# Kernel tuning notes

Hardware: AMD Instinct MI355X
Metric: run time of the kernel (lower is better)

The kernel has to match this reference:

```python
import jax, jax.numpy as jnp
import numpy as np

FEAT = 256
NUM_ATOMS = np.array([2048, 1536, 1024, 2048, 512, 1792, 1280, 2048], dtype=np.int32)
B = len(NUM_ATOMS)
N = int(NUM_ATOMS.sum())          # 12288 total atoms
MAXN = int(NUM_ATOMS.max())       # 2048
# Static segment bookkeeping (num_atoms is structural, not data)
_OFFSETS = np.concatenate([[0], np.cumsum(NUM_ATOMS)[:-1]])
SEG = np.repeat(np.arange(B), NUM_ATOMS)            # [N] graph id per atom
POS = np.arange(N) - _OFFSETS[SEG]                  # [N] position within graph
VALID = np.arange(MAXN)[None, :] < NUM_ATOMS[:, None]  # [B, MAXN] key mask


def setup_inputs() -> dict:
    key = jax.random.key(0)
    k1, k2 = jax.random.split(key)
    s = jax.random.normal(k1, (N, FEAT), jnp.float32)
    # dense: feat_dim -> 3*feat_dim, with bias
    W = jax.random.normal(k2, (FEAT, 3 * FEAT), jnp.float32) / np.float32(np.sqrt(FEAT))
    b = jnp.zeros((3 * FEAT,), jnp.float32)
    num_atoms = jnp.asarray(NUM_ATOMS)
    return {"s": s, "W": W, "b": b, "num_atoms": num_atoms}


def _pad(X):
    # scatter flat [N, FEAT] atoms into padded [B, MAXN, FEAT]
    return jnp.zeros((B, MAXN, FEAT), X.dtype).at[SEG, POS].set(X)


def reference(s, W, b, num_atoms):
    qkv = s @ W + b                          # [N, 3*FEAT]
    Q, K, V = jnp.split(qkv, 3, axis=-1)     # each [N, FEAT]
    Qp, Kp, Vp = _pad(Q), _pad(K), _pad(V)   # [B, MAXN, FEAT]
    scale = np.float32(1.0 / np.sqrt(FEAT))
    scores = jnp.einsum('bqd,bkd->bqk', Qp, Kp) * scale   # [B, MAXN, MAXN]
    scores = jnp.where(VALID[:, None, :], scores, -jnp.inf)  # mask padded keys
    att = jax.nn.softmax(scores, axis=-1)
    out = jnp.einsum('bqk,bkd->bqd', att, Vp)             # [B, MAXN, FEAT]
    return out[SEG, POS]                                   # back to flat [N, FEAT]
```

## Files before the change

### kernel.cpp

```cpp
#include <hip/hip_runtime.h>

typedef __attribute__((ext_vector_type(8))) short short8;
typedef __attribute__((ext_vector_type(4))) short s16x4;
typedef __attribute__((ext_vector_type(4))) float f32x4;

#define MFMA16(a,b,c) __builtin_amdgcn_mfma_f32_16x16x32_bf16((a),(b),(c),0,0,0)

__device__ __forceinline__ ushort f2bf(float f){ union{float f; unsigned u;} v; v.f=f; unsigned r=v.u + 0x7fffu + ((v.u>>16)&1u); return (ushort)(r>>16); }
__device__ __forceinline__ float bf2f(ushort u){ union{unsigned u; float f;} v; v.u = ((unsigned)u)<<16; return v.f; }

__global__ void __launch_bounds__(256) prep(const float* __restrict__ S,
    ushort* __restrict__ Sb, const float* __restrict__ W, ushort* __restrict__ Wt)
{
    __shared__ __align__(16) ushort tile[64*72];
    const int t = threadIdx.x;
    if (blockIdx.x < 1024){
        const int tid = blockIdx.x*256 + t;
#pragma unroll
        for (int r=0;r<3;r++){
            const int idx = tid + r*262144;
            f32x4 v = ((const f32x4*)S)[idx];
            s16x4 o;
            o[0]=(short)f2bf(v[0]); o[1]=(short)f2bf(v[1]);
            o[2]=(short)f2bf(v[2]); o[3]=(short)f2bf(v[3]);
            ((s16x4*)Sb)[idx] = o;
        }
    } else {
        const int i = blockIdx.x - 1024;
        const int r0 = (i&3)*64, c0 = (i>>2)*64;
        const int rr = t>>2, g = (t&3)*16;
        const float* sp = W + (size_t)(r0+rr)*768 + c0 + g;
#pragma unroll
        for (int j=0;j<16;j++) tile[(g+j)*72 + rr] = f2bf(sp[j]);
        __syncthreads();
        ushort* dp = Wt + (size_t)(c0+rr)*256 + r0 + g;
        *(short8*)dp     = *(const short8*)&tile[rr*72 + g];
        *(short8*)(dp+8) = *(const short8*)&tile[rr*72 + g + 8];
    }
}

__global__ void __launch_bounds__(256) qkv_gemm(const ushort* __restrict__ Sb,
    const ushort* __restrict__ Wt, const float* __restrict__ bias,
    ushort* __restrict__ Q, ushort* __restrict__ K, ushort* __restrict__ Vt)
{
    __shared__ __align__(16) ushort Bl[64*264];
    const int t = threadIdx.x, w = t>>6, l = t&63, lr = l&15, lq = l>>4;
    const int m0 = blockIdx.x*128, n0 = blockIdx.y*64;

#pragma unroll
    for (int s=0;s<8;s++){
        const int u = t + s*256, row = u>>5, c8 = u&31;
        *(short8*)&Bl[row*264 + c8*8] = *(const short8*)(Wt + (size_t)(n0+row)*256 + c8*8);
    }
    __syncthreads();

    if (n0 < 512){
        f32x4 acc[2][4];
#pragma unroll
        for (int a=0;a<2;a++)
#pragma unroll
            for (int b2=0;b2<4;b2++) acc[a][b2]=(f32x4){0.f,0.f,0.f,0.f};
        const ushort* ap = Sb + (size_t)(m0 + w*32 + lr)*256 + lq*8;
#pragma unroll
        for (int kc=0;kc<8;kc++){
            short8 af0 = *(const short8*)(ap + kc*32);
            short8 af1 = *(const short8*)(ap + 16*256 + kc*32);
#pragma unroll
            for (int nt=0;nt<4;nt++){
                short8 bf = *(const short8*)&Bl[(nt*16+lr)*264 + lq*8 + kc*32];
                acc[0][nt] = MFMA16(af0, bf, acc[0][nt]);
                acc[1][nt] = MFMA16(af1, bf, acc[1][nt]);
            }
        }
        ushort* dst = (n0 < 256) ? Q : K;
        const int colbase = n0 & 255;
#pragma unroll
        for (int nt=0;nt<4;nt++){
            float bv = bias[n0 + nt*16 + lr];
#pragma unroll
            for (int mt=0;mt<2;mt++){
                const int row = m0 + w*32 + mt*16 + lq*4;
                ushort* o = dst + (size_t)row*256 + colbase + nt*16 + lr;
#pragma unroll
                for (int i=0;i<4;i++) o[(size_t)i*256] = f2bf(acc[mt][nt][i] + bv);
            }
        }
    } else {
        const int f0 = n0 - 512;
        f32x4 acc[4][2];
#pragma unroll
        for (int a=0;a<4;a++)
#pragma unroll
            for (int b2=0;b2<2;b2++) acc[a][b2]=(f32x4){0.f,0.f,0.f,0.f};
        const ushort* bp = Sb + (size_t)(m0 + w*32 + lr)*256 + lq*8;
#pragma unroll
        for (int kc=0;kc<8;kc++){
            short8 bf0 = *(const short8*)(bp + kc*32);
            short8 bf1 = *(const short8*)(bp + 16*256 + kc*32);
#pragma unroll
            for (int ft=0;ft<4;ft++){
                short8 af = *(const short8*)&Bl[(ft*16+lr)*264 + lq*8 + kc*32];
                acc[ft][0] = MFMA16(af, bf0, acc[ft][0]);
                acc[ft][1] = MFMA16(af, bf1, acc[ft][1]);
            }
        }
#pragma unroll
        for (int ft=0;ft<4;ft++){
#pragma unroll
            for (int at=0;at<2;at++){
                ushort* o = Vt + (size_t)(f0 + ft*16 + lq*4)*12288 + m0 + w*32 + at*16 + lr;
#pragma unroll
                for (int i=0;i<4;i++){
                    float bv = bias[512 + f0 + ft*16 + lq*4 + i];
                    o[(size_t)i*12288] = f2bf(acc[ft][at][i] + bv);
                }
            }
        }
    }
}

template<int MODE>
__global__ void __launch_bounds__(256,2) attn_partial(const ushort* __restrict__ Qb,
    const ushort* __restrict__ Kb, const ushort* __restrict__ Vt,
    void* __restrict__ Optr, float* __restrict__ Lptr)
{
    __shared__ __align__(16) ushort Kl[32*264];
    __shared__ __align__(16) ushort Vl[256*40];
    __shared__ __align__(16) ushort Pl[4][32*40];
    const int t = threadIdx.x, w = t>>6, l = t&63, lr = l&15, lq = l>>4;

    const int offs[9]    = {0,2048,3584,4608,6656,7168,8960,10240,12288};
    const int pbase_t[8] = {0,8192,12800,14848,23040,23552,30720,34560};
    int bi = blockIdx.x, q0=0, kstart=0, kend=0, off=0, nbg=0, pbase=0;
#pragma unroll
    for (int s=0;s<8;s++){
        const int nb = offs[s+1]-offs[s];
        const int tiles = nb>>7, pieces = (nb+511)>>9;
        const int items = tiles*pieces;
        if (bi >= 0 && bi < items){
            const int tile = bi / pieces, piece = bi - tile*pieces;
            q0 = offs[s] + tile*128;
            kstart = offs[s] + piece*512;
            kend = min(offs[s]+nb, kstart+512);
            off = offs[s]; nbg = nb; pbase = pbase_t[s];
        }
        bi -= items;
    }
    const int nchunks = (kend - kstart) >> 5;
    const int pc = (kstart - off) >> 9;

    short8 qf[2][8];
#pragma unroll
    for (int g=0;g<2;g++){
        const ushort* qp = Qb + (size_t)(q0 + w*32 + g*16 + lr)*256 + lq*8;
#pragma unroll
        for (int kc=0;kc<8;kc++) qf[g][kc] = *(const short8*)(qp + kc*32);
    }
    f32x4 Oa[2][16];
#pragma unroll
    for (int g=0;g<2;g++)
#pragma unroll
        for (int ft=0;ft<16;ft++) Oa[g][ft] = (f32x4){0.f,0.f,0.f,0.f};
    float l_lane[2][4] = {{0.f,0.f,0.f,0.f},{0.f,0.f,0.f,0.f}};

    const int kr = t>>5, kcol = t&31;
    const ushort* kg0 = Kb + (size_t)(kstart + kr)*256 + kcol*8;
    const ushort* vg0 = Vt + (size_t)t*12288 + kstart;
    short8 kreg[4], vreg[4];
#pragma unroll
    for (int s=0;s<4;s++){
        kreg[s] = *(const short8*)(kg0 + (size_t)s*8*256);
        vreg[s] = *(const short8*)(vg0 + s*8);
    }

    for (int ck=0; ck<nchunks; ck++){
#pragma unroll
        for (int s=0;s<4;s++)
            *(short8*)&Kl[(kr + s*8)*264 + kcol*8] = kreg[s];
#pragma unroll
        for (int s=0;s<4;s++)
            *(short8*)&Vl[t*40 + s*8] = vreg[s];
        if (ck+1 < nchunks){
            const ushort* kg = kg0 + (size_t)(ck+1)*32*256;
            const ushort* vg = vg0 + (ck+1)*32;
#pragma unroll
            for (int s=0;s<4;s++){
                kreg[s] = *(const short8*)(kg + (size_t)s*8*256);
                vreg[s] = *(const short8*)(vg + s*8);
            }
        }
        __asm__ volatile("s_waitcnt lgkmcnt(0)" ::: "memory");
        __builtin_amdgcn_s_barrier();

        f32x4 sc[2][2];
#pragma unroll
        for (int g=0;g<2;g++)
#pragma unroll
            for (int h=0;h<2;h++) sc[g][h] = (f32x4){0.f,0.f,0.f,0.f};
        __builtin_amdgcn_s_setprio(1);
#pragma unroll
        for (int kc=0;kc<8;kc++){
            short8 b0 = *(const short8*)&Kl[ lr     *264 + kc*32 + lq*8];
            short8 b1 = *(const short8*)&Kl[(16+lr)*264 + kc*32 + lq*8];
#pragma unroll
            for (int g=0;g<2;g++){
                sc[g][0] = MFMA16(qf[g][kc], b0, sc[g][0]);
                sc[g][1] = MFMA16(qf[g][kc], b1, sc[g][1]);
            }
        }
        __builtin_amdgcn_s_setprio(0);
        ushort* pw = &Pl[w][0];
#pragma unroll
        for (int g=0;g<2;g++)
#pragma unroll
            for (int i=0;i<4;i++){
                float p0 = exp2f(sc[g][0][i]*0.0901684284f);
                float p1 = exp2f(sc[g][1][i]*0.0901684284f);
                l_lane[g][i] += p0 + p1;
                pw[(g*16+lq*4+i)*40 + lr]      = f2bf(p0);
                pw[(g*16+lq*4+i)*40 + 16 + lr] = f2bf(p1);
            }
        __asm__ volatile("s_waitcnt lgkmcnt(0)" ::: "memory");
        short8 pf0 = *(const short8*)&pw[ lr     *40 + lq*8];
        short8 pf1 = *(const short8*)&pw[(16+lr)*40 + lq*8];

        __builtin_amdgcn_s_setprio(1);
#pragma unroll
        for (int ft=0;ft<16;ft++){
            short8 vf = *(const short8*)&Vl[(ft*16+lr)*40 + lq*8];
            Oa[0][ft] = MFMA16(pf0, vf, Oa[0][ft]);
            Oa[1][ft] = MFMA16(pf1, vf, Oa[1][ft]);
        }
        __builtin_amdgcn_s_setprio(0);
        __builtin_amdgcn_s_barrier();
    }

#pragma unroll
    for (int g=0;g<2;g++)
#pragma unroll
        for (int i=0;i<4;i++){
            float r = l_lane[g][i];
            r += __shfl_xor(r,1); r += __shfl_xor(r,2);
            r += __shfl_xor(r,4); r += __shfl_xor(r,8);
            l_lane[g][i] = r;
        }

    if constexpr (MODE == 0){
        ushort* Op = (ushort*)Optr;
        const int prow0 = pbase + pc*nbg + (q0 + w*32 - off);
#pragma unroll
        for (int g=0;g<2;g++)
#pragma unroll
            for (int i=0;i<4;i++){
                ushort* o = Op + (size_t)(prow0 + g*16 + lq*4 + i)*256 + lr;
#pragma unroll
                for (int ft=0;ft<16;ft++) o[ft*16] = f2bf(Oa[g][ft][i]);
            }
        if (lr == 0){
#pragma unroll
            for (int g=0;g<2;g++)
#pragma unroll
                for (int i=0;i<4;i++)
                    Lptr[prow0 + g*16 + lq*4 + i] = l_lane[g][i];
        }
    } else {
        float* out = (float*)Optr;
#pragma unroll
        for (int g=0;g<2;g++){
            float* op = out + (size_t)(q0 + w*32 + g*16 + lq*4)*256 + lr;
#pragma unroll
            for (int i=0;i<4;i++)
#pragma unroll
                for (int ft=0;ft<16;ft++)
                    atomicAdd(&op[(size_t)i*256 + ft*16], Oa[g][ft][i]);
        }
        if (lr == 0){
#pragma unroll
            for (int g=0;g<2;g++)
#pragma unroll
                for (int i=0;i<4;i++)
                    atomicAdd(&Lptr[q0 + w*32 + g*16 + lq*4 + i], l_lane[g][i]);
        }
    }
}

__global__ void __launch_bounds__(256) reduce_norm(const ushort* __restrict__ Opart,
    const float* __restrict__ Lpart, float* __restrict__ out)
{
    const int offs[9]    = {0,2048,3584,4608,6656,7168,8960,10240,12288};
    const int pbase_t[8] = {0,8192,12800,14848,23040,23552,30720,34560};
    const int pieces_t[8]= {4,3,2,4,1,4,3,4};
    const int t = threadIdx.x;
    const int row = blockIdx.x*8 + (t>>5);
    const int f = (t&31)*8;
    int s = 0;
#pragma unroll
    for (int i=0;i<8;i++) if (row >= offs[i+1]) s = i+1;
    const int nb = offs[s+1]-offs[s], S = pieces_t[s];
    const int base = pbase_t[s] + (row - offs[s]);
    float acc[8] = {0.f,0.f,0.f,0.f,0.f,0.f,0.f,0.f};
    float L = 0.f;
    for (int p=0; p<S; p++){
        const size_t pr = (size_t)(base + p*nb);
        L += Lpart[pr];
        short8 v = *(const short8*)&Opart[pr*256 + f];
#pragma unroll
        for (int j=0;j<8;j++) acc[j] += bf2f((ushort)v[j]);
    }
    const float inv = 1.0f / L;
    f32x4 o0, o1;
#pragma unroll
    for (int j=0;j<4;j++){ o0[j] = acc[j]*inv; o1[j] = acc[4+j]*inv; }
    float* op = out + (size_t)row*256 + f;
    *(f32x4*)op     = o0;
    *(f32x4*)(op+4) = o1;
}

__global__ void __launch_bounds__(256) normalize_out(float* __restrict__ out,
    const float* __restrict__ lsum)
{
    const int row = blockIdx.x, t = threadIdx.x;
    const float inv = 1.0f / lsum[row];
    out[(size_t)row*256 + t] *= inv;
}

extern "C" void kernel_launch(void* const* d_in, const int* in_sizes, int n_in,
                              void* d_out, int out_size, void* d_ws, size_t ws_size,
                              hipStream_t stream)
{
    const float* S    = nullptr;
    const float* W    = nullptr;
    const float* bias = nullptr;
    for (int i = 0; i < n_in; i++){
        if      (in_sizes[i] == 3145728) S    = (const float*)d_in[i];
        else if (in_sizes[i] ==  196608) W    = (const float*)d_in[i];
        else if (in_sizes[i] ==     768) bias = (const float*)d_in[i];
    }
    if (!S)    S    = (const float*)d_in[0];
    if (!W)    W    = (const float*)d_in[1];
    if (!bias) bias = (const float*)d_in[2];

    float* out = (float*)d_out;

    ushort* ws  = (ushort*)d_ws;
    ushort* Wt  = ws;
    ushort* Qb  = Wt + 768*256;
    ushort* Kb  = Qb + 12288*256;
    ushort* Vtb = Kb + 12288*256;

    const size_t base_b  = ((size_t)768*256 + 3*(size_t)12288*256) * 2;
    const size_t opart_b = (size_t)42752*256*2;
    const size_t lpart_b = (size_t)42752*4;
    const bool mode0 = (ws_size >= base_b + opart_b + lpart_b);

    ushort* Sb = (ushort*)d_out;

    prep     <<<1072,        256, 0, stream>>>(S, Sb, W, Wt);
    qkv_gemm <<<dim3(96,12), 256, 0, stream>>>(Sb, Wt, bias, Qb, Kb, Vtb);

    if (mode0){
        ushort* Opart = (ushort*)((char*)d_ws + base_b);
        float*  Lpart = (float*)((char*)d_ws + base_b + opart_b);
        attn_partial<0><<<334, 256, 0, stream>>>(Qb, Kb, Vtb, (void*)Opart, Lpart);
        reduce_norm    <<<1536, 256, 0, stream>>>(Opart, Lpart, out);
    } else {
        float* lsum = (float*)((char*)d_ws + base_b);
        (void)hipMemsetAsync(d_out, 0, (size_t)12288*256*4, stream);
        (void)hipMemsetAsync(lsum,  0, (size_t)12288*4,     stream);
        attn_partial<1><<<334, 256, 0, stream>>>(Qb, Kb, Vtb, (void*)out, lsum);
        normalize_out  <<<12288, 256, 0, stream>>>(out, lsum);
    }
}
```

Before: 171.2 us.

## Split attention keys into 256-wide pieces and preload GEMM A fragments

The attention key range per block is now a template parameter. When the workspace is large enough, keys are split into 256-key pieces, which raises the grid from 334 to 644 blocks for better CU occupancy, at the cost of more partial outputs for reduce_norm to read and sum. The QKV GEMM now loads all A fragments into registers before the shared-memory staging of W, so those global loads overlap the staging. The manual waitcnt/barrier pairs and s_setprio hints are replaced with plain __syncthreads().

```diff
diff --git a/kernel.cpp b/kernel.cpp
--- a/kernel.cpp
+++ b/kernel.cpp
@@ -47,6 +47,14 @@
     const int t = threadIdx.x, w = t>>6, l = t&63, lr = l&15, lq = l>>4;
     const int m0 = blockIdx.x*128, n0 = blockIdx.y*64;
 
+    const ushort* ap = Sb + (size_t)(m0 + w*32 + lr)*256 + lq*8;
+    short8 sa[2][8];
+#pragma unroll
+    for (int g=0;g<2;g++)
+#pragma unroll
+        for (int kc=0;kc<8;kc++)
+            sa[g][kc] = *(const short8*)(ap + g*16*256 + kc*32);
+
 #pragma unroll
     for (int s=0;s<8;s++){
         const int u = t + s*256, row = u>>5, c8 = u&31;
@@ -60,16 +68,13 @@
         for (int a=0;a<2;a++)
 #pragma unroll
             for (int b2=0;b2<4;b2++) acc[a][b2]=(f32x4){0.f,0.f,0.f,0.f};
-        const ushort* ap = Sb + (size_t)(m0 + w*32 + lr)*256 + lq*8;
 #pragma unroll
         for (int kc=0;kc<8;kc++){
-            short8 af0 = *(const short8*)(ap + kc*32);
-            short8 af1 = *(const short8*)(ap + 16*256 + kc*32);
 #pragma unroll
             for (int nt=0;nt<4;nt++){
                 short8 bf = *(const short8*)&Bl[(nt*16+lr)*264 + lq*8 + kc*32];
-                acc[0][nt] = MFMA16(af0, bf, acc[0][nt]);
-                acc[1][nt] = MFMA16(af1, bf, acc[1][nt]);
+                acc[0][nt] = MFMA16(sa[0][kc], bf, acc[0][nt]);
+                acc[1][nt] = MFMA16(sa[1][kc], bf, acc[1][nt]);
             }
         }
         ushort* dst = (n0 < 256) ? Q : K;
@@ -92,16 +97,13 @@
         for (int a=0;a<4;a++)
 #pragma unroll
             for (int b2=0;b2<2;b2++) acc[a][b2]=(f32x4){0.f,0.f,0.f,0.f};
-        const ushort* bp = Sb + (size_t)(m0 + w*32 + lr)*256 + lq*8;
 #pragma unroll
         for (int kc=0;kc<8;kc++){
-            short8 bf0 = *(const short8*)(bp + kc*32);
-            short8 bf1 = *(const short8*)(bp + 16*256 + kc*32);
 #pragma unroll
             for (int ft=0;ft<4;ft++){
                 short8 af = *(const short8*)&Bl[(ft*16+lr)*264 + lq*8 + kc*32];
-                acc[ft][0] = MFMA16(af, bf0, acc[ft][0]);
-                acc[ft][1] = MFMA16(af, bf1, acc[ft][1]);
+                acc[ft][0] = MFMA16(af, sa[0][kc], acc[ft][0]);
+                acc[ft][1] = MFMA16(af, sa[1][kc], acc[ft][1]);
             }
         }
 #pragma unroll
@@ -119,7 +121,7 @@
     }
 }
 
-template<int MODE>
+template<int MODE, int PL>
 __global__ void __launch_bounds__(256,2) attn_partial(const ushort* __restrict__ Qb,
     const ushort* __restrict__ Kb, const ushort* __restrict__ Vt,
     void* __restrict__ Optr, float* __restrict__ Lptr)
@@ -128,26 +130,27 @@
     __shared__ __align__(16) ushort Vl[256*40];
     __shared__ __align__(16) ushort Pl[4][32*40];
     const int t = threadIdx.x, w = t>>6, l = t&63, lr = l&15, lq = l>>4;
-
-    const int offs[9]    = {0,2048,3584,4608,6656,7168,8960,10240,12288};
-    const int pbase_t[8] = {0,8192,12800,14848,23040,23552,30720,34560};
-    int bi = blockIdx.x, q0=0, kstart=0, kend=0, off=0, nbg=0, pbase=0;
+    constexpr int PIECE = 1 << PL;
+
+    const int offs[9] = {0,2048,3584,4608,6656,7168,8960,10240,12288};
+    int bi = blockIdx.x, q0=0, kstart=0, kend=0, off=0, nbg=0, pbase=0, pb=0;
 #pragma unroll
     for (int s=0;s<8;s++){
         const int nb = offs[s+1]-offs[s];
-        const int tiles = nb>>7, pieces = (nb+511)>>9;
+        const int tiles = nb>>7, pieces = (nb + PIECE-1)>>PL;
         const int items = tiles*pieces;
         if (bi >= 0 && bi < items){
             const int tile = bi / pieces, piece = bi - tile*pieces;
             q0 = offs[s] + tile*128;
-            kstart = offs[s] + piece*512;
-            kend = min(offs[s]+nb, kstart+512);
-            off = offs[s]; nbg = nb; pbase = pbase_t[s];
+            kstart = offs[s] + piece*PIECE;
+            kend = min(offs[s]+nb, kstart+PIECE);
+            off = offs[s]; nbg = nb; pbase = pb;
         }
         bi -= items;
+        pb += nb*pieces;
     }
     const int nchunks = (kend - kstart) >> 5;
-    const int pc = (kstart - off) >> 9;
+    const int pc = (kstart - off) >> PL;
 
     short8 qf[2][8];
 #pragma unroll
@@ -189,15 +192,13 @@
                 vreg[s] = *(const short8*)(vg + s*8);
             }
         }
-        __asm__ volatile("s_waitcnt lgkmcnt(0)" ::: "memory");
-        __builtin_amdgcn_s_barrier();
+        __syncthreads();
 
         f32x4 sc[2][2];
 #pragma unroll
         for (int g=0;g<2;g++)
 #pragma unroll
             for (int h=0;h<2;h++) sc[g][h] = (f32x4){0.f,0.f,0.f,0.f};
-        __builtin_amdgcn_s_setprio(1);
 #pragma unroll
         for (int kc=0;kc<8;kc++){
             short8 b0 = *(const short8*)&Kl[ lr     *264 + kc*32 + lq*8];
@@ -208,7 +209,6 @@
                 sc[g][1] = MFMA16(qf[g][kc], b1, sc[g][1]);
             }
         }
-        __builtin_amdgcn_s_setprio(0);
         ushort* pw = &Pl[w][0];
 #pragma unroll
         for (int g=0;g<2;g++)
@@ -224,15 +224,13 @@
         short8 pf0 = *(const short8*)&pw[ lr     *40 + lq*8];
         short8 pf1 = *(const short8*)&pw[(16+lr)*40 + lq*8];
 
-        __builtin_amdgcn_s_setprio(1);
 #pragma unroll
         for (int ft=0;ft<16;ft++){
             short8 vf = *(const short8*)&Vl[(ft*16+lr)*40 + lq*8];
             Oa[0][ft] = MFMA16(pf0, vf, Oa[0][ft]);
             Oa[1][ft] = MFMA16(pf1, vf, Oa[1][ft]);
         }
-        __builtin_amdgcn_s_setprio(0);
-        __builtin_amdgcn_s_barrier();
+        __syncthreads();
     }
 
 #pragma unroll
@@ -285,19 +283,24 @@
 }
 
 __global__ void __launch_bounds__(256) reduce_norm(const ushort* __restrict__ Opart,
-    const float* __restrict__ Lpart, float* __restrict__ out)
-{
-    const int offs[9]    = {0,2048,3584,4608,6656,7168,8960,10240,12288};
-    const int pbase_t[8] = {0,8192,12800,14848,23040,23552,30720,34560};
-    const int pieces_t[8]= {4,3,2,4,1,4,3,4};
+    const float* __restrict__ Lpart, float* __restrict__ out, int PL)
+{
+    const int offs[9] = {0,2048,3584,4608,6656,7168,8960,10240,12288};
     const int t = threadIdx.x;
     const int row = blockIdx.x*8 + (t>>5);
     const int f = (t&31)*8;
-    int s = 0;
-#pragma unroll
-    for (int i=0;i<8;i++) if (row >= offs[i+1]) s = i+1;
-    const int nb = offs[s+1]-offs[s], S = pieces_t[s];
-    const int base = pbase_t[s] + (row - offs[s]);
+    const int PIECE = 1 << PL;
+    int s = 0, pbase = 0, pb = 0, nb = 0, S = 0, base = 0;
+#pragma unroll
+    for (int i=0;i<8;i++){
+        const int nbi = offs[i+1]-offs[i];
+        const int pieces = (nbi + PIECE-1) >> PL;
+        if (row >= offs[i] && row < offs[i+1]){
+            nb = nbi; S = pieces; pbase = pb; base = pb + (row - offs[i]);
+        }
+        pb += nbi*pieces;
+    }
+    (void)pbase; (void)s;
     float acc[8] = {0.f,0.f,0.f,0.f,0.f,0.f,0.f,0.f};
     float L = 0.f;
     for (int p=0; p<S; p++){
@@ -348,26 +351,30 @@
     ushort* Kb  = Qb + 12288*256;
     ushort* Vtb = Kb + 12288*256;
 
-    const size_t base_b  = ((size_t)768*256 + 3*(size_t)12288*256) * 2;
-    const size_t opart_b = (size_t)42752*256*2;
-    const size_t lpart_b = (size_t)42752*4;
-    const bool mode0 = (ws_size >= base_b + opart_b + lpart_b);
+    const size_t base_b = ((size_t)768*256 + 3*(size_t)12288*256) * 2;
+    const size_t need256 = base_b + (size_t)82432*512 + (size_t)82432*4;
+    const size_t need512 = base_b + (size_t)42752*512 + (size_t)42752*4;
 
     ushort* Sb = (ushort*)d_out;
 
     prep     <<<1072,        256, 0, stream>>>(S, Sb, W, Wt);
     qkv_gemm <<<dim3(96,12), 256, 0, stream>>>(Sb, Wt, bias, Qb, Kb, Vtb);
 
-    if (mode0){
+    if (ws_size >= need256){
         ushort* Opart = (ushort*)((char*)d_ws + base_b);
-        float*  Lpart = (float*)((char*)d_ws + base_b + opart_b);
-        attn_partial<0><<<334, 256, 0, stream>>>(Qb, Kb, Vtb, (void*)Opart, Lpart);
-        reduce_norm    <<<1536, 256, 0, stream>>>(Opart, Lpart, out);
+        float*  Lpart = (float*)((char*)d_ws + base_b + (size_t)82432*512);
+        attn_partial<0,8><<<644, 256, 0, stream>>>(Qb, Kb, Vtb, (void*)Opart, Lpart);
+        reduce_norm      <<<1536, 256, 0, stream>>>(Opart, Lpart, out, 8);
+    } else if (ws_size >= need512){
+        ushort* Opart = (ushort*)((char*)d_ws + base_b);
+        float*  Lpart = (float*)((char*)d_ws + base_b + (size_t)42752*512);
+        attn_partial<0,9><<<334, 256, 0, stream>>>(Qb, Kb, Vtb, (void*)Opart, Lpart);
+        reduce_norm      <<<1536, 256, 0, stream>>>(Opart, Lpart, out, 9);
     } else {
         float* lsum = (float*)((char*)d_ws + base_b);
         (void)hipMemsetAsync(d_out, 0, (size_t)12288*256*4, stream);
         (void)hipMemsetAsync(lsum,  0, (size_t)12288*4,     stream);
-        attn_partial<1><<<334, 256, 0, stream>>>(Qb, Kb, Vtb, (void*)out, lsum);
-        normalize_out  <<<12288, 256, 0, stream>>>(out, lsum);
-    }
-}
+        attn_partial<1,9><<<334, 256, 0, stream>>>(Qb, Kb, Vtb, (void*)out, lsum);
+        normalize_out    <<<12288, 256, 0, stream>>>(out, lsum);
+    }
+}
```

After: 184.1 us. 7.5% more time.
